# Kernel optimization log

Measured on AMD Instinct MI355X. Metric: run time of the kernel, lower is better.

The kernel has to match this reference:

```python
import jax, jax.numpy as jnp
import numpy as np

H = 64        # num_attention_heads
HK = 8        # num_key_value_heads
HD = 64       # head_dim
DM = 1024     # hidden_size
WINDOW = 128  # sliding_window


def setup_inputs() -> dict:
    key = jax.random.key(0)
    ks = jax.random.split(key, 9)
    B, S = 2, 1024
    s = 0.02
    return {
        "x": jax.random.normal(ks[0], (B, S, DM), jnp.float32),
        "Wq": jax.random.normal(ks[1], (H * HD, DM), jnp.float32) * s,
        "bq": jax.random.normal(ks[2], (H * HD,), jnp.float32) * s,
        "Wk": jax.random.normal(ks[3], (HK * HD, DM), jnp.float32) * s,
        "bk": jax.random.normal(ks[4], (HK * HD,), jnp.float32) * s,
        "Wv": jax.random.normal(ks[5], (HK * HD, DM), jnp.float32) * s,
        "bv": jax.random.normal(ks[6], (HK * HD,), jnp.float32) * s,
        "Wo": jax.random.normal(ks[7], (DM, H * HD), jnp.float32) * s,
        "bo": jax.random.normal(ks[8], (DM,), jnp.float32) * s,
        "sinks": jnp.ones((H,), jnp.float32),
    }


def reference(x, Wq, bq, Wk, bk, Wv, bv, Wo, bo, sinks):
    B, S, _ = x.shape
    G = H // HK  # GQA group size

    q = (x @ Wq.T + bq).reshape(B, S, H, HD).transpose(0, 2, 1, 3)    # [B,H,S,hd]
    k = (x @ Wk.T + bk).reshape(B, S, HK, HD).transpose(0, 2, 1, 3)   # [B,Hk,S,hd]
    v = (x @ Wv.T + bv).reshape(B, S, HK, HD).transpose(0, 2, 1, 3)
    k = jnp.repeat(k, G, axis=1)  # [B,H,S,hd]
    v = jnp.repeat(v, G, axis=1)

    scale = 1.0 / np.sqrt(HD).astype(np.float32)
    scores = jnp.einsum("bhqd,bhkd->bhqk", q, k) * scale  # [B,H,S,S]

    # causal + sliding-window mask: attend iff 0 <= q_pos - k_pos < WINDOW
    qi = jnp.arange(S)[:, None]
    kj = jnp.arange(S)[None, :]
    allowed = (qi >= kj) & (qi - kj < WINDOW)             # [S,S]
    neg = jnp.asarray(-1e30, scores.dtype)
    scores = jnp.where(allowed[None, None], scores, neg)

    # per-head learned sink logit appended as an extra softmax column
    sink = jnp.broadcast_to(sinks[None, :, None, None], (B, H, S, 1))
    logits = jnp.concatenate([scores, sink], axis=-1)      # [B,H,S,S+1]
    probs = jax.nn.softmax(logits, axis=-1)[..., :-1]      # drop sink column

    o = jnp.einsum("bhqk,bhkd->bhqd", probs, v)            # [B,H,S,hd]
    o = o.transpose(0, 2, 1, 3).reshape(B, S, H * HD)
    return o @ Wo.T + bo                                   # [B,S,DM]
```

## Files before the change

kernel.cpp:

```cpp
#include <hip/hip_runtime.h>
#include <math.h>

#define H 64
#define HK 8
#define HD 64
#define DM 1024
#define WINDOW 128
#define GQA (H / HK)
#define Bv 2
#define Sv 1024

typedef _Float16 f16;
typedef __attribute__((ext_vector_type(8))) _Float16 f16x8;
typedef __attribute__((ext_vector_type(4))) _Float16 f16x4;
typedef __attribute__((ext_vector_type(4))) float f32x4;

__device__ __forceinline__ void gload_lds16(const void* g, void* l) {
    __builtin_amdgcn_global_load_lds((const __attribute__((address_space(1))) void*)g,
                                     (__attribute__((address_space(3))) void*)l, 16, 0, 0);
}

template <int MODE>
__device__ __forceinline__ void gemm_body(const f16* __restrict__ A,
                                          const f16* __restrict__ W,
                                          const float* __restrict__ bias,
                                          void* __restrict__ outp,
                                          int bx, int by, int N, int K, int lda,
                                          f16* As, f16* Bs) {
    const int t    = threadIdx.x;
    const int lane = t & 63;
    const int w    = t >> 6;
    const int wm   = w >> 1;
    const int wn   = w & 1;
    const int lr   = lane & 15;
    const int quad = lane >> 4;
    const int m0   = by * 128;
    const int n0   = bx * 128;

    const int srow = lane >> 3;
    const int gsw  = lane & 7;

    f32x4 acc[4][4] = {};

    for (int k0 = 0; k0 < K; k0 += 64) {
#pragma unroll
        for (int i = 0; i < 4; ++i) {
            const int row = (w * 4 + i) * 8 + srow;
            const int g   = gsw ^ (row & 7);
            gload_lds16(A + (size_t)(m0 + row) * lda + k0 + g * 8, As + (w * 4 + i) * 512);
            gload_lds16(W + (size_t)(n0 + row) * lda + k0 + g * 8, Bs + (w * 4 + i) * 512);
        }
        __syncthreads();
#pragma unroll
        for (int ks = 0; ks < 2; ++ks) {
            f16x8 af[4], bf[4];
#pragma unroll
            for (int tt = 0; tt < 4; ++tt) {
                const int m  = wm * 64 + tt * 16 + lr;
                const int ca = (ks * 4 + quad) ^ (m & 7);
                af[tt] = *(const f16x8*)(As + m * 64 + ca * 8);
                const int n  = wn * 64 + tt * 16 + lr;
                const int cb = (ks * 4 + quad) ^ (n & 7);
                bf[tt] = *(const f16x8*)(Bs + n * 64 + cb * 8);
            }
#pragma unroll
            for (int i = 0; i < 4; ++i)
#pragma unroll
                for (int j = 0; j < 4; ++j)
                    acc[i][j] = __builtin_amdgcn_mfma_f32_16x16x32_f16(af[i], bf[j], acc[i][j], 0, 0, 0);
        }
        __syncthreads();
    }

#pragma unroll
    for (int i = 0; i < 4; ++i) {
        const int grow = m0 + wm * 64 + i * 16 + quad * 4;
#pragma unroll
        for (int j = 0; j < 4; ++j) {
            const int gcol = n0 + wn * 64 + j * 16 + lr;
            if (MODE == 1) {
                const float bz = bias[gcol];
#pragma unroll
                for (int r = 0; r < 4; ++r)
                    ((f16*)outp)[(size_t)(grow + r) * N + gcol] = (f16)(acc[i][j][r] + bz);
            } else if (MODE == 2) {
                const float bz = bias[gcol];
                const int lc = gcol & 511;
                const size_t base = (size_t)(grow >> 10) * 524288 + (size_t)(lc >> 6) * 65536
                                  + (size_t)(grow & 1023) * 64 + (lc & 63);
#pragma unroll
                for (int r = 0; r < 4; ++r)
                    ((f16*)outp)[base + (size_t)r * 64] = (f16)(acc[i][j][r] + bz);
            } else if (MODE == 3) {
                const float bz = bias[gcol];
                const int lc = gcol & 511;
                const size_t base = ((size_t)(grow >> 10) * 512 + lc) * 1024 + (grow & 1023);
                f16x4 o;
#pragma unroll
                for (int r = 0; r < 4; ++r) o[r] = (f16)(acc[i][j][r] + bz);
                *(f16x4*)((f16*)outp + base) = o;
            } else {
#pragma unroll
                for (int r = 0; r < 4; ++r)
                    ((float*)outp)[(size_t)(grow + r) * N + gcol] = acc[i][j][r];
            }
        }
    }
}

__global__ __launch_bounds__(256) void qkv_gemm(const f16* __restrict__ xh,
                                                const f16* __restrict__ Wf,
                                                const float* __restrict__ bf,
                                                f16* __restrict__ qh,
                                                f16* __restrict__ khb,
                                                f16* __restrict__ vtb) {
    __shared__ __align__(16) f16 As[128 * 64];
    __shared__ __align__(16) f16 Bs[128 * 64];
    const int bx = blockIdx.x, by = blockIdx.y;
    if (bx < 32)
        gemm_body<1>(xh, Wf, bf, qh, bx, by, H * HD, DM, DM, As, Bs);
    else if (bx < 36)
        gemm_body<2>(xh, Wf, bf, khb, bx, by, 0, DM, DM, As, Bs);
    else
        gemm_body<3>(xh, Wf, bf, vtb, bx, by, 0, DM, DM, As, Bs);
}

__global__ __launch_bounds__(256) void o_gemm_split(const f16* __restrict__ oh,
                                                    const f16* __restrict__ Woh,
                                                    float* __restrict__ partials) {
    __shared__ __align__(16) f16 As[128 * 64];
    __shared__ __align__(16) f16 Bs[128 * 64];
    const int kz = blockIdx.z;
    gemm_body<4>(oh + kz * 1024, Woh + kz * 1024, nullptr,
                 partials + (size_t)kz * 2097152,
                 blockIdx.x, blockIdx.y, DM, 1024, H * HD, As, Bs);
}

__global__ __launch_bounds__(256) void reduce4(const float* __restrict__ partials,
                                               const float* __restrict__ bo,
                                               float* __restrict__ out) {
    const int i = blockIdx.x * 256 + threadIdx.x;
    const float4* p = (const float4*)partials;
    float4 a = p[i];
    float4 b1 = p[i + 524288], b2 = p[i + 1048576], b3 = p[i + 1572864];
    float4 bz = ((const float4*)bo)[i & 255];
    float4 o;
    o.x = a.x + b1.x + b2.x + b3.x + bz.x;
    o.y = a.y + b1.y + b2.y + b3.y + bz.y;
    o.z = a.z + b1.z + b2.z + b3.z + bz.z;
    o.w = a.w + b1.w + b2.w + b3.w + bz.w;
    ((float4*)out)[i] = o;
}

#define C_X  524288
#define C_WQ 1572864
#define C_WK 1703936
#define C_WV 1835008
#define C_WO 2883584

__global__ __launch_bounds__(256) void convert_all(const float* __restrict__ x,
                                                   const float* __restrict__ Wq,
                                                   const float* __restrict__ Wk,
                                                   const float* __restrict__ Wv,
                                                   const float* __restrict__ Wo,
                                                   f16* __restrict__ xh,
                                                   f16* __restrict__ wqkv,
                                                   f16* __restrict__ woh) {
    const int i = blockIdx.x * 256 + threadIdx.x;
    const float* src;
    f16* dst;
    int off;
    if (i < C_X)       { src = x;  dst = xh;              off = i; }
    else if (i < C_WQ) { src = Wq; dst = wqkv;            off = i - C_X; }
    else if (i < C_WK) { src = Wk; dst = wqkv + 4194304;  off = i - C_WQ; }
    else if (i < C_WV) { src = Wv; dst = wqkv + 4718592;  off = i - C_WK; }
    else               { src = Wo; dst = woh;             off = i - C_WV; }
    const float4 v = ((const float4*)src)[off];
    f16x4 o;
    o[0] = (f16)v.x; o[1] = (f16)v.y; o[2] = (f16)v.z; o[3] = (f16)v.w;
    *(f16x4*)(dst + (size_t)off * 4) = o;
}

__global__ __launch_bounds__(256) void build_bias(const float* __restrict__ bq,
                                                  const float* __restrict__ bk,
                                                  const float* __restrict__ bv,
                                                  float* __restrict__ bf) {
    const int i = blockIdx.x * 256 + threadIdx.x;
    float v;
    if (i < 4096)      v = bq[i];
    else if (i < 4608) v = bk[i - 4096];
    else               v = bv[i - 4608];
    bf[i] = v;
}

#define KT 192
#define KLS 72
#define VTS 200
#define PLS 200

__global__ __launch_bounds__(256) void attn_mfma(const f16* __restrict__ qh,
                                                 const f16* __restrict__ khb,
                                                 const f16* __restrict__ vtb,
                                                 const float* __restrict__ sinks,
                                                 f16* __restrict__ oh) {
    __shared__ __align__(16) f16 Kl[KT * KLS];
    __shared__ __align__(16) f16 Vt[HD * VTS];
    __shared__ __align__(16) f16 Pl[4 * 16 * PLS];

    const int t  = threadIdx.x;
    const int q0 = blockIdx.x * 64;
    const int hk = blockIdx.y >> 1;
    const int hh = blockIdx.y & 1;
    const int b  = blockIdx.z;
    const int c0 = q0 - WINDOW;

    const f16* kg = khb + (size_t)(b * HK + hk) * Sv * HD;
    const f16* vg = vtb + (size_t)(b * HK + hk) * HD * Sv;

#pragma unroll
    for (int ii = 0; ii < 6; ++ii) {
        const int i = ii * 256 + t;
        const int slot = i >> 3, c = i & 7;
        const int j = c0 + slot;
        f16x8 val = {};
        if (j >= 0) val = *(const f16x8*)(kg + (size_t)j * HD + c * 8);
        *(f16x8*)(&Kl[slot * KLS + c * 8]) = val;
    }
#pragma unroll
    for (int ii = 0; ii < 6; ++ii) {
        const int i = ii * 256 + t;
        const int d = i / 24, c = i % 24;
        const int j0 = c0 + c * 8;
        f16x8 val = {};
        if (j0 >= 0) val = *(const f16x8*)(vg + (size_t)d * Sv + j0);
        *(f16x8*)(&Vt[d * VTS + c * 8]) = val;
    }
    __syncthreads();

    const int lane = t & 63;
    const int w    = t >> 6;
    const int h    = hk * GQA + hh * 4 + w;
    const int lr   = lane & 15;
    const int quad = lane >> 4;
    f16* Pw = Pl + w * 16 * PLS;

    f16x8 qf[4][2];
#pragma unroll
    for (int mt = 0; mt < 4; ++mt) {
        const int q = q0 + mt * 16 + lr;
        const f16* qrow = qh + (size_t)(b * Sv + q) * (H * HD) + h * HD;
#pragma unroll
        for (int ks = 0; ks < 2; ++ks)
            qf[mt][ks] = *(const f16x8*)(qrow + ks * 32 + quad * 8);
    }
    const float sk   = sinks[h];
    const int   smin = (c0 < 0) ? -c0 : 0;
    const float scale = 0.125f;

#pragma unroll
    for (int mt = 0; mt < 4; ++mt) {
        f32x4 S[12];
#pragma unroll
        for (int nt = 0; nt < 12; ++nt) {
            f32x4 a = {};
#pragma unroll
            for (int ks = 0; ks < 2; ++ks) {
                f16x8 bfr = *(const f16x8*)(&Kl[(nt * 16 + lr) * KLS + ks * 32 + quad * 8]);
                a = __builtin_amdgcn_mfma_f32_16x16x32_f16(qf[mt][ks], bfr, a, 0, 0, 0);
            }
            S[nt] = a;
        }
        float rmax[4] = {-1e30f, -1e30f, -1e30f, -1e30f};
#pragma unroll
        for (int nt = 0; nt < 12; ++nt) {
            const int sl = nt * 16 + lr;
#pragma unroll
            for (int r = 0; r < 4; ++r) {
                const int mq = mt * 16 + quad * 4 + r;
                const bool ok = (sl > mq) && (sl <= mq + WINDOW) && (sl >= smin);
                const float v = ok ? S[nt][r] * scale : -INFINITY;
                S[nt][r] = v;
                rmax[r] = fmaxf(rmax[r], v);
            }
        }
#pragma unroll
        for (int off = 1; off < 16; off <<= 1)
#pragma unroll
            for (int r = 0; r < 4; ++r)
                rmax[r] = fmaxf(rmax[r], __shfl_xor(rmax[r], off, 64));
        float mrow[4], lsum[4];
#pragma unroll
        for (int r = 0; r < 4; ++r) { mrow[r] = fmaxf(rmax[r], sk); lsum[r] = 0.f; }
#pragma unroll
        for (int nt = 0; nt < 12; ++nt) {
#pragma unroll
            for (int r = 0; r < 4; ++r) {
                const float p = __expf(S[nt][r] - mrow[r]);
                lsum[r] += p;
                Pw[(quad * 4 + r) * PLS + nt * 16 + lr] = (f16)p;
            }
        }
#pragma unroll
        for (int off = 1; off < 16; off <<= 1)
#pragma unroll
            for (int r = 0; r < 4; ++r)
                lsum[r] += __shfl_xor(lsum[r], off, 64);
        float inv[4];
#pragma unroll
        for (int r = 0; r < 4; ++r)
            inv[r] = 1.f / (lsum[r] + __expf(sk - mrow[r]));
        f32x4 O[4] = {};
#pragma unroll
        for (int kc = 0; kc < 6; ++kc) {
            const f16x8 pa = *(const f16x8*)(&Pw[lr * PLS + kc * 32 + quad * 8]);
#pragma unroll
            for (int dt = 0; dt < 4; ++dt) {
                const f16x8 vf = *(const f16x8*)(&Vt[(dt * 16 + lr) * VTS + kc * 32 + quad * 8]);
                O[dt] = __builtin_amdgcn_mfma_f32_16x16x32_f16(pa, vf, O[dt], 0, 0, 0);
            }
        }
#pragma unroll
        for (int dt = 0; dt < 4; ++dt) {
#pragma unroll
            for (int r = 0; r < 4; ++r) {
                const int q = q0 + mt * 16 + quad * 4 + r;
                oh[(size_t)(b * Sv + q) * (H * HD) + h * HD + dt * 16 + lr] =
                    (f16)(O[dt][r] * inv[r]);
            }
        }
    }
}

extern "C" void kernel_launch(void* const* d_in, const int* in_sizes, int n_in,
                              void* d_out, int out_size, void* d_ws, size_t ws_size,
                              hipStream_t stream) {
    const float* x     = (const float*)d_in[0];
    const float* Wq    = (const float*)d_in[1];
    const float* bq    = (const float*)d_in[2];
    const float* Wk    = (const float*)d_in[3];
    const float* bk    = (const float*)d_in[4];
    const float* Wv    = (const float*)d_in[5];
    const float* bv    = (const float*)d_in[6];
    const float* Wo    = (const float*)d_in[7];
    const float* bo    = (const float*)d_in[8];
    const float* sinks = (const float*)d_in[9];
    float* out = (float*)d_out;

    f16* xh   = (f16*)d_ws;
    f16* wqkv = xh + 2097152;
    f16* qh   = wqkv + 5242880;
    f16* khb  = qh + 8388608;
    f16* vtb  = khb + 1048576;
    f16* woh  = vtb + 1048576;
    f16* oh   = woh + 4194304;
    float* bqkv = (float*)(oh + 8388608);
    float* partials = (float*)d_ws;

    convert_all<<<dim3(C_WO / 256), dim3(256), 0, stream>>>(x, Wq, Wk, Wv, Wo, xh, wqkv, woh);
    build_bias<<<dim3(20), dim3(256), 0, stream>>>(bq, bk, bv, bqkv);

    qkv_gemm<<<dim3(40, 16), dim3(256), 0, stream>>>(xh, wqkv, bqkv, qh, khb, vtb);

    attn_mfma<<<dim3(Sv / 64, HK * 2, Bv), dim3(256), 0, stream>>>(qh, khb, vtb, sinks, oh);

    o_gemm_split<<<dim3(8, 16, 4), dim3(256), 0, stream>>>(oh, woh, partials);
    reduce4<<<dim3(2048), dim3(256), 0, stream>>>(partials, bo, out);
}
```

Before: 204.0 us.

## Retile QKV GEMM to 128x160 tiles, fold scale and bias build

```diff
diff --git a/kernel.cpp b/kernel.cpp
--- a/kernel.cpp
+++ b/kernel.cpp
@@ -20,35 +20,132 @@
                                      (__attribute__((address_space(3))) void*)l, 16, 0, 0);
 }
 
-template <int MODE>
-__device__ __forceinline__ void gemm_body(const f16* __restrict__ A,
-                                          const f16* __restrict__ W,
-                                          const float* __restrict__ bias,
-                                          void* __restrict__ outp,
-                                          int bx, int by, int N, int K, int lda,
-                                          f16* As, f16* Bs) {
+__global__ __launch_bounds__(256, 2) void qkv_gemm(const f16* __restrict__ xh,
+                                                   const f16* __restrict__ wqkv,
+                                                   const float* __restrict__ bqkv,
+                                                   f16* __restrict__ qh,
+                                                   f16* __restrict__ khb,
+                                                   f16* __restrict__ vtb) {
+    __shared__ __align__(16) f16 As[128 * 64];
+    __shared__ __align__(16) f16 Bs[160 * 64];
+
     const int t    = threadIdx.x;
     const int lane = t & 63;
     const int w    = t >> 6;
+    const int lr   = lane & 15;
+    const int quad = lane >> 4;
+    const int srow = lane >> 3;
+    const int gsw  = lane & 7;
+    const int bx   = blockIdx.x & 31;
+    const int by   = blockIdx.x >> 5;
+    const int m0   = by * 128;
+    const int n0   = bx * 160;
     const int wm   = w >> 1;
     const int wn   = w & 1;
-    const int lr   = lane & 15;
-    const int quad = lane >> 4;
-    const int m0   = by * 128;
-    const int n0   = bx * 128;
-
-    const int srow = lane >> 3;
-    const int gsw  = lane & 7;
-
-    f32x4 acc[4][4] = {};
-
-    for (int k0 = 0; k0 < K; k0 += 64) {
+
+    f32x4 acc[4][5] = {};
+
+    for (int k0 = 0; k0 < DM; k0 += 64) {
 #pragma unroll
         for (int i = 0; i < 4; ++i) {
             const int row = (w * 4 + i) * 8 + srow;
             const int g   = gsw ^ (row & 7);
-            gload_lds16(A + (size_t)(m0 + row) * lda + k0 + g * 8, As + (w * 4 + i) * 512);
-            gload_lds16(W + (size_t)(n0 + row) * lda + k0 + g * 8, Bs + (w * 4 + i) * 512);
+            gload_lds16(xh + (size_t)(m0 + row) * DM + k0 + g * 8, As + (w * 4 + i) * 512);
+        }
+#pragma unroll
+        for (int i = 0; i < 5; ++i) {
+            const int row = (w * 5 + i) * 8 + srow;
+            const int g   = gsw ^ (row & 7);
+            gload_lds16(wqkv + (size_t)(n0 + row) * DM + k0 + g * 8, Bs + (w * 5 + i) * 512);
+        }
+        __syncthreads();
+#pragma unroll
+        for (int ks = 0; ks < 2; ++ks) {
+            f16x8 af[4], bf[5];
+#pragma unroll
+            for (int tt = 0; tt < 4; ++tt) {
+                const int m  = wm * 64 + tt * 16 + lr;
+                const int ca = (ks * 4 + quad) ^ (m & 7);
+                af[tt] = *(const f16x8*)(As + m * 64 + ca * 8);
+            }
+#pragma unroll
+            for (int tt = 0; tt < 5; ++tt) {
+                const int n  = wn * 80 + tt * 16 + lr;
+                const int cb = (ks * 4 + quad) ^ (n & 7);
+                bf[tt] = *(const f16x8*)(Bs + n * 64 + cb * 8);
+            }
+#pragma unroll
+            for (int i = 0; i < 4; ++i)
+#pragma unroll
+                for (int j = 0; j < 5; ++j)
+                    acc[i][j] = __builtin_amdgcn_mfma_f32_16x16x32_f16(af[i], bf[j], acc[i][j], 0, 0, 0);
+        }
+        __syncthreads();
+    }
+
+#pragma unroll
+    for (int i = 0; i < 4; ++i) {
+        const int grow = m0 + wm * 64 + i * 16 + quad * 4;
+#pragma unroll
+        for (int j = 0; j < 5; ++j) {
+            const int gcb  = n0 + wn * 80 + j * 16;
+            const int gcol = gcb + lr;
+            const float bz = bqkv[gcol];
+            if (gcb < 4096) {
+#pragma unroll
+                for (int r = 0; r < 4; ++r)
+                    qh[(size_t)(grow + r) * 4096 + gcol] = (f16)((acc[i][j][r] + bz) * 0.125f);
+            } else if (gcb < 4608) {
+                const int lc = gcol - 4096;
+                const size_t base = (size_t)(grow >> 10) * 524288 + (size_t)(lc >> 6) * 65536
+                                  + (size_t)(grow & 1023) * 64 + (lc & 63);
+#pragma unroll
+                for (int r = 0; r < 4; ++r)
+                    khb[base + (size_t)r * 64] = (f16)(acc[i][j][r] + bz);
+            } else {
+                const int lc = gcol - 4608;
+                const size_t base = ((size_t)(grow >> 10) * 512 + lc) * 1024 + (grow & 1023);
+                f16x4 o;
+#pragma unroll
+                for (int r = 0; r < 4; ++r) o[r] = (f16)(acc[i][j][r] + bz);
+                *(f16x4*)(vtb + base) = o;
+            }
+        }
+    }
+}
+
+__global__ __launch_bounds__(256, 2) void o_gemm_split(const f16* __restrict__ oh,
+                                                       const f16* __restrict__ woh,
+                                                       float* __restrict__ partials) {
+    __shared__ __align__(16) f16 As[128 * 64];
+    __shared__ __align__(16) f16 Bs[128 * 64];
+
+    const int t    = threadIdx.x;
+    const int lane = t & 63;
+    const int w    = t >> 6;
+    const int lr   = lane & 15;
+    const int quad = lane >> 4;
+    const int srow = lane >> 3;
+    const int gsw  = lane & 7;
+    const int kz   = blockIdx.z;
+    const int m0   = blockIdx.y * 128;
+    const int n0   = blockIdx.x * 128;
+    const int wm   = w >> 1;
+    const int wn   = w & 1;
+
+    const f16* A = oh  + (size_t)kz * 1024;
+    const f16* W = woh + (size_t)kz * 1024;
+    float* P = partials + (size_t)kz * 2097152;
+
+    f32x4 acc[4][4] = {};
+
+    for (int k0 = 0; k0 < 1024; k0 += 64) {
+#pragma unroll
+        for (int i = 0; i < 4; ++i) {
+            const int row = (w * 4 + i) * 8 + srow;
+            const int g   = gsw ^ (row & 7);
+            gload_lds16(A + (size_t)(m0 + row) * 4096 + k0 + g * 8, As + (w * 4 + i) * 512);
+            gload_lds16(W + (size_t)(n0 + row) * 4096 + k0 + g * 8, Bs + (w * 4 + i) * 512);
         }
         __syncthreads();
 #pragma unroll
@@ -78,62 +175,11 @@
 #pragma unroll
         for (int j = 0; j < 4; ++j) {
             const int gcol = n0 + wn * 64 + j * 16 + lr;
-            if (MODE == 1) {
-                const float bz = bias[gcol];
-#pragma unroll
-                for (int r = 0; r < 4; ++r)
-                    ((f16*)outp)[(size_t)(grow + r) * N + gcol] = (f16)(acc[i][j][r] + bz);
-            } else if (MODE == 2) {
-                const float bz = bias[gcol];
-                const int lc = gcol & 511;
-                const size_t base = (size_t)(grow >> 10) * 524288 + (size_t)(lc >> 6) * 65536
-                                  + (size_t)(grow & 1023) * 64 + (lc & 63);
-#pragma unroll
-                for (int r = 0; r < 4; ++r)
-                    ((f16*)outp)[base + (size_t)r * 64] = (f16)(acc[i][j][r] + bz);
-            } else if (MODE == 3) {
-                const float bz = bias[gcol];
-                const int lc = gcol & 511;
-                const size_t base = ((size_t)(grow >> 10) * 512 + lc) * 1024 + (grow & 1023);
-                f16x4 o;
-#pragma unroll
-                for (int r = 0; r < 4; ++r) o[r] = (f16)(acc[i][j][r] + bz);
-                *(f16x4*)((f16*)outp + base) = o;
-            } else {
-#pragma unroll
-                for (int r = 0; r < 4; ++r)
-                    ((float*)outp)[(size_t)(grow + r) * N + gcol] = acc[i][j][r];
-            }
-        }
-    }
-}
-
-__global__ __launch_bounds__(256) void qkv_gemm(const f16* __restrict__ xh,
-                                                const f16* __restrict__ Wf,
-                                                const float* __restrict__ bf,
-                                                f16* __restrict__ qh,
-                                                f16* __restrict__ khb,
-                                                f16* __restrict__ vtb) {
-    __shared__ __align__(16) f16 As[128 * 64];
-    __shared__ __align__(16) f16 Bs[128 * 64];
-    const int bx = blockIdx.x, by = blockIdx.y;
-    if (bx < 32)
-        gemm_body<1>(xh, Wf, bf, qh, bx, by, H * HD, DM, DM, As, Bs);
-    else if (bx < 36)
-        gemm_body<2>(xh, Wf, bf, khb, bx, by, 0, DM, DM, As, Bs);
-    else
-        gemm_body<3>(xh, Wf, bf, vtb, bx, by, 0, DM, DM, As, Bs);
-}
-
-__global__ __launch_bounds__(256) void o_gemm_split(const f16* __restrict__ oh,
-                                                    const f16* __restrict__ Woh,
-                                                    float* __restrict__ partials) {
-    __shared__ __align__(16) f16 As[128 * 64];
-    __shared__ __align__(16) f16 Bs[128 * 64];
-    const int kz = blockIdx.z;
-    gemm_body<4>(oh + kz * 1024, Woh + kz * 1024, nullptr,
-                 partials + (size_t)kz * 2097152,
-                 blockIdx.x, blockIdx.y, DM, 1024, H * HD, As, Bs);
+#pragma unroll
+            for (int r = 0; r < 4; ++r)
+                P[(size_t)(grow + r) * 1024 + gcol] = acc[i][j][r];
+        }
+    }
 }
 
 __global__ __launch_bounds__(256) void reduce4(const float* __restrict__ partials,
@@ -141,7 +187,7 @@
                                                float* __restrict__ out) {
     const int i = blockIdx.x * 256 + threadIdx.x;
     const float4* p = (const float4*)partials;
-    float4 a = p[i];
+    float4 a  = p[i];
     float4 b1 = p[i + 524288], b2 = p[i + 1048576], b3 = p[i + 1572864];
     float4 bz = ((const float4*)bo)[i & 255];
     float4 o;
@@ -163,10 +209,21 @@
                                                    const float* __restrict__ Wk,
                                                    const float* __restrict__ Wv,
                                                    const float* __restrict__ Wo,
+                                                   const float* __restrict__ bq,
+                                                   const float* __restrict__ bk,
+                                                   const float* __restrict__ bv,
                                                    f16* __restrict__ xh,
                                                    f16* __restrict__ wqkv,
-                                                   f16* __restrict__ woh) {
+                                                   f16* __restrict__ woh,
+                                                   float* __restrict__ bqkv) {
     const int i = blockIdx.x * 256 + threadIdx.x;
+    if (i < 5120) {
+        float v;
+        if (i < 4096)      v = bq[i];
+        else if (i < 4608) v = bk[i - 4096];
+        else               v = bv[i - 4608];
+        bqkv[i] = v;
+    }
     const float* src;
     f16* dst;
     int off;
@@ -181,18 +238,6 @@
     *(f16x4*)(dst + (size_t)off * 4) = o;
 }
 
-__global__ __launch_bounds__(256) void build_bias(const float* __restrict__ bq,
-                                                  const float* __restrict__ bk,
-                                                  const float* __restrict__ bv,
-                                                  float* __restrict__ bf) {
-    const int i = blockIdx.x * 256 + threadIdx.x;
-    float v;
-    if (i < 4096)      v = bq[i];
-    else if (i < 4608) v = bk[i - 4096];
-    else               v = bv[i - 4608];
-    bf[i] = v;
-}
-
 #define KT 192
 #define KLS 72
 #define VTS 200
@@ -255,7 +300,6 @@
     }
     const float sk   = sinks[h];
     const int   smin = (c0 < 0) ? -c0 : 0;
-    const float scale = 0.125f;
 
 #pragma unroll
     for (int mt = 0; mt < 4; ++mt) {
@@ -278,7 +322,7 @@
             for (int r = 0; r < 4; ++r) {
                 const int mq = mt * 16 + quad * 4 + r;
                 const bool ok = (sl > mq) && (sl <= mq + WINDOW) && (sl >= smin);
-                const float v = ok ? S[nt][r] * scale : -INFINITY;
+                const float v = ok ? S[nt][r] : -INFINITY;
                 S[nt][r] = v;
                 rmax[r] = fmaxf(rmax[r], v);
             }
@@ -356,10 +400,10 @@
     float* bqkv = (float*)(oh + 8388608);
     float* partials = (float*)d_ws;
 
-    convert_all<<<dim3(C_WO / 256), dim3(256), 0, stream>>>(x, Wq, Wk, Wv, Wo, xh, wqkv, woh);
-    build_bias<<<dim3(20), dim3(256), 0, stream>>>(bq, bk, bv, bqkv);
-
-    qkv_gemm<<<dim3(40, 16), dim3(256), 0, stream>>>(xh, wqkv, bqkv, qh, khb, vtb);
+    convert_all<<<dim3(C_WO / 256), dim3(256), 0, stream>>>(
+        x, Wq, Wk, Wv, Wo, bq, bk, bv, xh, wqkv, woh, bqkv);
+
+    qkv_gemm<<<dim3(512), dim3(256), 0, stream>>>(xh, wqkv, bqkv, qh, khb, vtb);
 
     attn_mfma<<<dim3(Sv / 64, HK * 2, Bv), dim3(256), 0, stream>>>(qh, khb, vtb, sinks, oh);
 
```

New measurement: 182.6 us. -10.5%, faster.
